# Performance work log

Measured on AMD Instinct MI355X. Metric: run time of the kernel, lower is better.

## Reference

```python
import jax, jax.numpy as jnp
import numpy as np

B, S, D, H, HD, L, V, FF = 4, 2048, 768, 12, 64, 6, 32000, 3072
EPS = 1e-5


def setup_inputs() -> dict:
    key = jax.random.key(0)
    ks = jax.random.split(key, 12)
    s = 0.02
    return {
        "input_ids": jax.random.randint(ks[0], (B, S), 0, V),
        "emb": jax.random.normal(ks[1], (V, D), jnp.float32) * s,
        "q_w": jax.random.normal(ks[2], (L, D, D), jnp.float32) * s,
        "q_b": jnp.zeros((L, D), jnp.float32),
        "k_w": jax.random.normal(ks[3], (L, D, D), jnp.float32) * s,
        "k_b": jnp.zeros((L, D), jnp.float32),
        "v_w": jax.random.normal(ks[4], (L, D, D), jnp.float32) * s,
        "v_b": jnp.zeros((L, D), jnp.float32),
        "o_w": jax.random.normal(ks[5], (L, D, D), jnp.float32) * s,
        "o_b": jnp.zeros((L, D), jnp.float32),
        "f1_w": jax.random.normal(ks[6], (L, D, FF), jnp.float32) * s,
        "f1_b": jnp.zeros((L, FF), jnp.float32),
        "f2_w": jax.random.normal(ks[7], (L, FF, D), jnp.float32) * s,
        "f2_b": jnp.zeros((L, D), jnp.float32),
        "n1_w": jnp.ones((L, D), jnp.float32),
        "n1_b": jnp.zeros((L, D), jnp.float32),
        "n2_w": jnp.ones((L, D), jnp.float32),
        "n2_b": jnp.zeros((L, D), jnp.float32),
        "fn_w": jnp.ones((D,), jnp.float32),
        "fn_b": jnp.zeros((D,), jnp.float32),
    }


def _ln(x, w, b):
    m = jnp.mean(x, axis=-1, keepdims=True)
    v = jnp.var(x, axis=-1, keepdims=True)
    return (x - m) * jax.lax.rsqrt(v + EPS) * w + b


def _rope(x):
    # x: [B, S, D]; RoPE applied on full embed dim (as in source)
    inv_freq = 1.0 / (10000.0 ** (jnp.arange(0, D, 2, dtype=jnp.float32) / D))
    ang = jnp.arange(x.shape[1], dtype=jnp.float32)[:, None] * inv_freq[None, :]  # [S, D/2]
    cos, sin = jnp.cos(ang), jnp.sin(ang)
    xe, xo = x[..., ::2], x[..., 1::2]
    re = xe * cos - xo * sin
    ro = xo * cos + xe * sin
    return jnp.stack([re, ro], axis=-1).reshape(x.shape)


def _forward(input_ids, emb, q_w, q_b, k_w, k_b, v_w, v_b, o_w, o_b,
             f1_w, f1_b, f2_w, f2_b, n1_w, n1_b, n2_w, n2_b, fn_w, fn_b):
    h = _rope(emb[input_ids])  # [B, S, D]
    scale = 1.0 / np.sqrt(HD)

    def block(h, p):
        (qw, qb, kw, kb, vw, vb, ow, ob, f1w, f1b, f2w, f2b,
         w1, b1, w2, b2) = p
        xn = _ln(h, w1, b1)
        q = (xn @ qw + qb).reshape(B, S, H, HD)
        k = (xn @ kw + kb).reshape(B, S, H, HD)
        v = (xn @ vw + vb).reshape(B, S, H, HD)
        scores = jnp.einsum('bqhd,bkhd->bhqk', q, k) * scale
        attn = jax.nn.softmax(scores, axis=-1)
        ctx = jnp.einsum('bhqk,bkhd->bqhd', attn, v).reshape(B, S, D)
        h = h + (ctx @ ow + ob)
        xn2 = _ln(h, w2, b2)
        ff = jax.nn.gelu(xn2 @ f1w + f1b, approximate=False) @ f2w + f2b
        return h + ff, None

    params = (q_w, q_b, k_w, k_b, v_w, v_b, o_w, o_b,
              f1_w, f1_b, f2_w, f2_b, n1_w, n1_b, n2_w, n2_b)
    h, _ = jax.lax.scan(block, h, params)
    h = _ln(h, fn_w, fn_b)
    return h @ emb.T  # tied output projection: [B, S, V]


def reference(input_ids, emb, q_w, q_b, k_w, k_b, v_w, v_b, o_w, o_b,
              f1_w, f1_b, f2_w, f2_b, n1_w, n1_b, n2_w, n2_b, fn_w, fn_b):
    return _forward(input_ids, emb, q_w, q_b, k_w, k_b, v_w, v_b, o_w, o_b,
                    f1_w, f1_b, f2_w, f2_b, n1_w, n1_b, n2_w, n2_b, fn_w, fn_b)
```

## Files before the change

### kernel.cpp

```cpp
#include <hip/hip_runtime.h>
#include <hip/hip_bf16.h>
#include <cstdint>
#include <cstddef>

#define TB 4
#define TS 2048
#define TD 768
#define TH 12
#define THD 64
#define TL 6
#define TV 32000
#define TFF 3072
#define TT (TB*TS)
#define TQKV 2304

typedef __bf16 bf16_t;
typedef __attribute__((ext_vector_type(8))) __bf16 bf16x8;
typedef __attribute__((ext_vector_type(4))) __bf16 bf16x4;
typedef __attribute__((ext_vector_type(4))) float f32x4;

__device__ __forceinline__ unsigned short f2bf(float f) {
  union { float f; unsigned u; } x; x.f = f;
  unsigned r = x.u + 0x7fffu + ((x.u >> 16) & 1u);
  return (unsigned short)(r >> 16);
}

__device__ __forceinline__ float fexp2(float x) {
  float r; asm("v_exp_f32 %0, %1" : "=v"(r) : "v"(x)); return r;
}

__device__ __forceinline__ void gld_lds16(const void* g, void* l) {
  unsigned loff = (unsigned)(uintptr_t)l;
  __builtin_amdgcn_global_load_lds(
      (const __attribute__((address_space(1))) unsigned int*)(uintptr_t)g,
      (__attribute__((address_space(3))) unsigned int*)(uintptr_t)loff, 16, 0, 0);
}

#define IRFENCE() asm volatile("" ::: "memory")

__global__ void embed_rope(const int* __restrict__ ids, const float* __restrict__ emb,
                           float* __restrict__ h) {
  int t = blockIdx.x;
  int s = t & (TS - 1);
  int id = ids[t];
  const float* row = emb + (size_t)id * TD;
  float* out = h + (size_t)t * TD;
  for (int p = threadIdx.x; p < TD/2; p += blockDim.x) {
    float xe = row[2*p], xo = row[2*p+1];
    float inv = expf(-(float)(2*p) * (9.210340371976184f / (float)TD));
    float ang = (float)s * inv;
    float c = cosf(ang), sn = sinf(ang);
    out[2*p]   = xe*c - xo*sn;
    out[2*p+1] = xo*c + xe*sn;
  }
}

__global__ __launch_bounds__(256) void ln_fwd(const float* __restrict__ x,
                                              const float* __restrict__ w,
                                              const float* __restrict__ b,
                                              unsigned short* __restrict__ y) {
  int row = blockIdx.x;
  const float* xr = x + (size_t)row * TD;
  int tid = threadIdx.x;
  float4 v = {0.f, 0.f, 0.f, 0.f};
  if (tid < 192) v = *(const float4*)(xr + tid*4);
  float s = (v.x+v.y)+(v.z+v.w);
  float q = (v.x*v.x+v.y*v.y)+(v.z*v.z+v.w*v.w);
  for (int o = 32; o; o >>= 1) { s += __shfl_down(s, o); q += __shfl_down(q, o); }
  __shared__ float ss[4], sq[4];
  int wave = tid >> 6, lane = tid & 63;
  if (lane == 0) { ss[wave] = s; sq[wave] = q; }
  __syncthreads();
  s = ss[0]+ss[1]+ss[2]+ss[3];
  q = sq[0]+sq[1]+sq[2]+sq[3];
  float mean = s * (1.0f/TD);
  float var  = q * (1.0f/TD) - mean*mean;
  float rstd = rsqrtf(var + 1e-5f);
  if (tid < 192) {
    const float4 wv = *(const float4*)(w + tid*4);
    const float4 bv = *(const float4*)(b + tid*4);
    ushort4 o4;
    o4.x = f2bf((v.x-mean)*rstd*wv.x + bv.x);
    o4.y = f2bf((v.y-mean)*rstd*wv.y + bv.y);
    o4.z = f2bf((v.z-mean)*rstd*wv.z + bv.z);
    o4.w = f2bf((v.w-mean)*rstd*wv.w + bv.w);
    *(ushort4*)(y + (size_t)row*TD + tid*4) = o4;
  }
}

__global__ __launch_bounds__(256) void transpose_to_bf16(const float* __restrict__ W,
                                                         unsigned short* __restrict__ Wt,
                                                         int K, int N, int row_off,
                                                         size_t lstride) {
  int ntn = N / 64;
  int tk = (blockIdx.x / ntn) * 64;
  int tn = (blockIdx.x % ntn) * 64;
  const float* Wb = W + (size_t)blockIdx.y * K * N;
  unsigned short* Ob = Wt + (size_t)blockIdx.y * lstride;
  __shared__ float tile[64][65];
  int tid = threadIdx.x;
  int c = tid & 63, w = tid >> 6;
  #pragma unroll
  for (int i = 0; i < 16; ++i) {
    int r = i*4 + w;
    tile[r][c] = Wb[(size_t)(tk + r) * N + tn + c];
  }
  __syncthreads();
  #pragma unroll
  for (int i = 0; i < 16; ++i) {
    int r = i*4 + w;
    Ob[(size_t)(row_off + tn + r) * K + tk + c] = f2bf(tile[c][r]);
  }
}

__global__ void pack_qkv_bias(const float* __restrict__ qb, const float* __restrict__ kb,
                              const float* __restrict__ vb, float* __restrict__ out) {
  int lay = blockIdx.x, i = threadIdx.x;
  out[lay*TQKV + i]        = qb[lay*TD + i];
  out[lay*TQKV + TD + i]   = kb[lay*TD + i];
  out[lay*TQKV + 2*TD + i] = vb[lay*TD + i];
}

__global__ void convert_bf16_k(const float* __restrict__ in, unsigned short* __restrict__ out) {
  size_t i = ((size_t)blockIdx.x * 256 + threadIdx.x) * 4;
  float4 v = *(const float4*)(in + i);
  ushort4 o;
  o.x = f2bf(v.x); o.y = f2bf(v.y); o.z = f2bf(v.z); o.w = f2bf(v.w);
  *(ushort4*)(out + i) = o;
}

template<int MODE>
__global__ __launch_bounds__(256, 2) void gemm_bt(
    const bf16_t* __restrict__ A, const bf16_t* __restrict__ Bt,
    const float* __restrict__ bias, void* __restrict__ out,
    void* __restrict__ out2,
    int N, int K, int ntn) {
  __shared__ __align__(16) bf16_t As[2][128*64];
  __shared__ __align__(16) bf16_t Bs[2][128*64];
  const int tid = threadIdx.x;
  const int lane = tid & 63;
  const int wave = tid >> 6;
  const int wm = wave >> 1, wn = wave & 1;
  const int nwg = gridDim.x;
  const int orig = blockIdx.x;
  const int qd = nwg >> 3, rr = nwg & 7;
  const int xcd = orig & 7, sub = orig >> 3;
  const int wg = (xcd < rr ? xcd*(qd+1) : rr*(qd+1) + (xcd-rr)*qd) + sub;
  const int tm = wg / ntn, tn = wg % ntn;
  const bf16_t* Ab = A + (size_t)tm * 128 * K;
  const bf16_t* Bb = Bt + (size_t)tn * 128 * K;
  const int lr = lane >> 3;
  const int lc = ((lane & 7) ^ lr) * 8;
  const int l15 = lane & 15, l4 = lane >> 4;
  const int flip = (l15 & 7) << 3;
  const int NT = K >> 6;
  f32x4 acc[4][4] = {};

#define STAGE(t, buf) do {                                                   \
    _Pragma("unroll")                                                        \
    for (int it = 0; it < 4; ++it) {                                         \
      const int r0 = it*32 + wave*8;                                         \
      gld_lds16(Ab + (size_t)(r0 + lr)*K + (t)*64 + lc, &As[buf][r0*64 + lr*64]); \
      gld_lds16(Bb + (size_t)(r0 + lr)*K + (t)*64 + lc, &Bs[buf][r0*64 + lr*64]); \
    }                                                                        \
  } while (0)

  STAGE(0, 0);
  for (int t = 0; t < NT; ++t) {
    const int cur = t & 1;
    if (t < NT - 1) {
      STAGE(t+1, cur^1);
      asm volatile("s_waitcnt vmcnt(8)" ::: "memory");
    } else {
      asm volatile("s_waitcnt vmcnt(0)" ::: "memory");
    }
    IRFENCE(); __builtin_amdgcn_s_barrier(); IRFENCE();
    #pragma unroll
    for (int kh = 0; kh < 2; ++kh) {
      bf16x8 af[4], bfr[4];
      #pragma unroll
      for (int i = 0; i < 4; ++i)
        af[i] = *(const bf16x8*)&As[cur][(wm*64 + i*16 + l15)*64 + ((kh*32 + l4*8) ^ flip)];
      #pragma unroll
      for (int i = 0; i < 4; ++i)
        bfr[i] = *(const bf16x8*)&Bs[cur][(wn*64 + i*16 + l15)*64 + ((kh*32 + l4*8) ^ flip)];
      #pragma unroll
      for (int mi = 0; mi < 4; ++mi)
        #pragma unroll
        for (int ni = 0; ni < 4; ++ni)
          acc[mi][ni] = __builtin_amdgcn_mfma_f32_16x16x32_bf16(af[mi], bfr[ni], acc[mi][ni], 0, 0, 0);
    }
    IRFENCE(); __builtin_amdgcn_s_barrier(); IRFENCE();
  }
#undef STAGE
  const int rb = tm*128 + wm*64 + l4*4;
  const int cbase = tn*128 + wn*64 + l15;
  const bool vsec = (MODE == 4) && (tn >= (2*TD)/128);
  #pragma unroll
  for (int mi = 0; mi < 4; ++mi) {
    #pragma unroll
    for (int ni = 0; ni < 4; ++ni) {
      const int c = cbase + ni*16;
      const float bv = (MODE == 3) ? 0.0f : bias[c];
      if (MODE == 4 && vsec) {
        const int cc = c - 2*TD;
        const int hh = cc >> 6, d = cc & 63;
        const int row0 = rb + mi*16;
        const int bidx = row0 >> 11, s = row0 & (TS-1);
        ushort4 o4;
        o4.x = f2bf(acc[mi][ni][0] + bv);
        o4.y = f2bf(acc[mi][ni][1] + bv);
        o4.z = f2bf(acc[mi][ni][2] + bv);
        o4.w = f2bf(acc[mi][ni][3] + bv);
        *(ushort4*)((unsigned short*)out2 + ((size_t)(bidx*TH + hh)*THD + d)*TS + s) = o4;
        continue;
      }
      #pragma unroll
      for (int r = 0; r < 4; ++r) {
        const size_t idx = (size_t)(rb + mi*16 + r) * N + c;
        float vv = acc[mi][ni][r] + bv;
        if (MODE == 0 || MODE == 4) {
          ((unsigned short*)out)[idx] = f2bf(vv);
        } else if (MODE == 1) {
          vv = 0.5f * vv * (1.0f + erff(vv * 0.70710678118654752f));
          ((unsigned short*)out)[idx] = f2bf(vv);
        } else if (MODE == 2) {
          ((float*)out)[idx] += vv;
        } else {
          ((float*)out)[idx] = vv;
        }
      }
    }
  }
}

__device__ __forceinline__ int lds_half_off(int R, int C) {
  int lin = ((((R >> 4) << 1) | (C >> 5)) << 10) | ((R & 15) << 6) | ((C & 31) << 1);
  return lin ^ (((R >> 3) & 1) << 5);
}

template<int MODE>
__global__ __launch_bounds__(512, 2) void gemm256(
    const bf16_t* __restrict__ A, const bf16_t* __restrict__ Bt,
    const float* __restrict__ bias, void* __restrict__ out,
    int N, int K, int ntn) {
  __shared__ __align__(16) bf16_t lds[2][2][2][8192];
  const int tid = threadIdx.x;
  const int lane = tid & 63;
  const int wave = tid >> 6;
  const int wm = wave >> 2;
  const int wn = wave & 3;
  const int orig = blockIdx.x;
  const int xcd = orig & 7, sub = orig >> 3;
  const int tm = xcd * 4 + (sub & 3);
  const int tn = sub >> 2;
  const bf16_t* Ab = A  + (size_t)tm * 256 * K;
  const bf16_t* Bb = Bt + (size_t)tn * 256 * K;
  const int l15 = lane & 15, l4 = lane >> 4;
  const int s_row = wave*16 + (lane >> 2);
  const int s_col0 = ((lane & 3) * 8) ^ ((lane >= 32) ? 16 : 0);
  const int NT = K >> 6;

  f32x4 acc[2][4][2][2] = {};
  bf16x8 afr[4][2], bfr0[2][2], bfr1[2][2];

#define STAGEH(mat, half, kt, buf) do {                                          \
    const bf16_t* base_ = (mat) ? Bb : Ab;                                       \
    _Pragma("unroll")                                                            \
    for (int j_ = 0; j_ < 2; ++j_)                                               \
      gld_lds16(base_ + (size_t)((half)*128 + s_row)*K + (kt)*64 + j_*32 + s_col0, \
                &lds[buf][mat][half][(wave*2 + j_) * 512]);                      \
  } while (0)
#define RDA(buf, half) do {                                                      \
    _Pragma("unroll")                                                            \
    for (int m4_ = 0; m4_ < 4; ++m4_)                                            \
      _Pragma("unroll")                                                          \
      for (int kh_ = 0; kh_ < 2; ++kh_)                                          \
        afr[m4_][kh_] = *(const bf16x8*)((const char*)&lds[buf][0][half][0] +    \
            lds_half_off(wm*64 + m4_*16 + l15, kh_*32 + l4*8));                  \
  } while (0)
#define RDB(buf, half, dst) do {                                                 \
    _Pragma("unroll")                                                            \
    for (int n2_ = 0; n2_ < 2; ++n2_)                                            \
      _Pragma("unroll")                                                          \
      for (int kh_ = 0; kh_ < 2; ++kh_)                                          \
        dst[n2_][kh_] = *(const bf16x8*)((const char*)&lds[buf][1][half][0] +    \
            lds_half_off(wn*32 + n2_*16 + l15, kh_*32 + l4*8));                  \
  } while (0)
#define MMA(hA, hB, bsrc) do {                                                   \
    __builtin_amdgcn_s_setprio(1);                                               \
    _Pragma("unroll")                                                            \
    for (int m4_ = 0; m4_ < 4; ++m4_)                                            \
      _Pragma("unroll")                                                          \
      for (int n2_ = 0; n2_ < 2; ++n2_)                                          \
        _Pragma("unroll")                                                        \
        for (int kh_ = 0; kh_ < 2; ++kh_)                                        \
          acc[hA][m4_][hB][n2_] = __builtin_amdgcn_mfma_f32_16x16x32_bf16(       \
              afr[m4_][kh_], bsrc[n2_][kh_], acc[hA][m4_][hB][n2_], 0, 0, 0);    \
    __builtin_amdgcn_s_setprio(0);                                               \
  } while (0)
#define WAITV(n)  asm volatile("s_waitcnt vmcnt(" #n ")" ::: "memory")
#define GATE()    do { asm volatile("s_waitcnt lgkmcnt(0)" ::: "memory");        \
                       __builtin_amdgcn_sched_barrier(0); } while (0)
#define BAR()     do { IRFENCE(); __builtin_amdgcn_s_barrier(); IRFENCE(); } while (0)

  STAGEH(0, 0, 0, 0);
  STAGEH(1, 0, 0, 0);
  STAGEH(1, 1, 0, 0);
  STAGEH(0, 1, 0, 0);
  WAITV(4);
  BAR();

  for (int t = 0; t < NT; ++t) {
    const int c = t & 1;
    const bool last = (t == NT - 1);
    RDA(c, 0);
    RDB(c, 0, bfr0);
    if (!last) STAGEH(0, 0, t+1, c^1);
    if (last) WAITV(2); else WAITV(4);
    BAR(); GATE();
    MMA(0, 0, bfr0);
    RDB(c, 1, bfr1);
    if (!last) STAGEH(1, 0, t+1, c^1);
    if (last) WAITV(0); else WAITV(4);
    BAR(); GATE();
    MMA(0, 1, bfr1);
    RDA(c, 1);
    if (!last) STAGEH(1, 1, t+1, c^1);
    BAR(); GATE();
    MMA(1, 0, bfr0);
    if (!last) STAGEH(0, 1, t+1, c^1);
    WAITV(4);
    BAR(); GATE();
    MMA(1, 1, bfr1);
  }

  #pragma unroll
  for (int hA = 0; hA < 2; ++hA)
    #pragma unroll
    for (int m4 = 0; m4 < 4; ++m4) {
      const int row = tm*256 + hA*128 + wm*64 + m4*16 + l4*4;
      #pragma unroll
      for (int hB = 0; hB < 2; ++hB)
        #pragma unroll
        for (int n2 = 0; n2 < 2; ++n2) {
          const int col = tn*256 + hB*128 + wn*32 + n2*16 + l15;
          const float bv = (MODE == 3) ? 0.0f : bias[col];
          #pragma unroll
          for (int r = 0; r < 4; ++r) {
            const size_t idx = (size_t)(row + r) * N + col;
            float vv = acc[hA][m4][hB][n2][r] + bv;
            if (MODE == 0) {
              ((unsigned short*)out)[idx] = f2bf(vv);
            } else if (MODE == 1) {
              vv = 0.5f * vv * (1.0f + erff(vv * 0.70710678118654752f));
              ((unsigned short*)out)[idx] = f2bf(vv);
            } else if (MODE == 2) {
              ((float*)out)[idx] += vv;
            } else {
              ((float*)out)[idx] = vv;
            }
          }
        }
    }
#undef STAGEH
#undef RDA
#undef RDB
#undef MMA
#undef WAITV
#undef GATE
#undef BAR
}

__global__ __launch_bounds__(256) void attn_fwd(
    const bf16_t* __restrict__ xqkv, const bf16_t* __restrict__ vt,
    unsigned short* __restrict__ ctx) {
  __shared__ __align__(16) bf16_t Ks[3][64*64];
  __shared__ __align__(16) bf16_t Vs[3][64*64];
  __shared__ __align__(16) bf16_t pl[4][32*64];
  const int tid = threadIdx.x, lane = tid & 63, wave = tid >> 6;
  const int orig = blockIdx.x;
  const int wg = (orig & 7) * 96 + (orig >> 3);
  const int qb16 = wg & 15;
  const int bh = wg >> 4;
  const int b = bh / TH, h = bh % TH;
  const bf16_t* qp = xqkv + (size_t)b*TS*TQKV + h*THD;
  const bf16_t* kp = xqkv + (size_t)b*TS*TQKV + TD + h*THD;
  const bf16_t* vp = vt + (size_t)bh*THD*TS;
  const int l15 = lane & 15, l4 = lane >> 4;
  const int qrow0 = qb16*128 + wave*32;
  const float C1 = 0.18033688011112042f;
  bf16x8 qf[2][2];
  #pragma unroll
  for (int mi = 0; mi < 2; ++mi)
    #pragma unroll
    for (int kh = 0; kh < 2; ++kh)
      qf[mi][kh] = *(const bf16x8*)(qp + (size_t)(qrow0 + mi*16 + l15)*TQKV + kh*32 + l4*8);
  const int srow = lane >> 3;
  const int scol = ((lane & 7) ^ srow) * 8;
  f32x4 o[2][4] = {};
  float rm[2] = {-1e30f, -1e30f}, rl[2] = {0.0f, 0.0f};
  const int flipw = (l15 & 7) << 3;

  #define STAGE(t, buf) do {                                                     \
    _Pragma("unroll")                                                            \
    for (int i_ = 0; i_ < 2; ++i_) {                                             \
      const int r_ = i_*32 + wave*8;                                             \
      gld_lds16(kp + (size_t)((t)*64 + r_ + srow)*TQKV + scol, &Ks[buf][r_*64]); \
      gld_lds16(vp + (size_t)(r_ + srow)*TS + (t)*64 + scol,   &Vs[buf][r_*64]); \
    }                                                                            \
  } while (0)

  STAGE(0, 0);
  STAGE(1, 1);
  int cur = 0;
  for (int t = 0; t < TS/64; ++t) {
    if (t < TS/64 - 1) {
      asm volatile("s_waitcnt vmcnt(4)" ::: "memory");
    } else {
      asm volatile("s_waitcnt vmcnt(0)" ::: "memory");
    }
    IRFENCE(); __builtin_amdgcn_s_barrier(); IRFENCE();
    if (t + 2 < TS/64) {
      const int nb = (cur + 2 >= 3) ? cur - 1 : cur + 2;
      STAGE(t+2, nb);
    }
    bf16x8 kf[4][2];
    #pragma unroll
    for (int nj = 0; nj < 4; ++nj) {
      const int row = nj*16 + l15;
      const int flip = (row & 7) << 3;
      #pragma unroll
      for (int kh = 0; kh < 2; ++kh)
        kf[nj][kh] = *(const bf16x8*)&Ks[cur][row*64 + ((kh*32 + l4*8) ^ flip)];
    }
    f32x4 st[2][4] = {};
    #pragma unroll
    for (int mi = 0; mi < 2; ++mi)
      #pragma unroll
      for (int nj = 0; nj < 4; ++nj) {
        st[mi][nj] = __builtin_amdgcn_mfma_f32_16x16x32_bf16(kf[nj][0], qf[mi][0], st[mi][nj], 0, 0, 0);
        st[mi][nj] = __builtin_amdgcn_mfma_f32_16x16x32_bf16(kf[nj][1], qf[mi][1], st[mi][nj], 0, 0, 0);
      }
    float mx[2];
    #pragma unroll
    for (int mi = 0; mi < 2; ++mi) {
      float m0 = fmaxf(fmaxf(st[mi][0][0], st[mi][0][1]), fmaxf(st[mi][0][2], st[mi][0][3]));
      float m1 = fmaxf(fmaxf(st[mi][1][0], st[mi][1][1]), fmaxf(st[mi][1][2], st[mi][1][3]));
      float m2 = fmaxf(fmaxf(st[mi][2][0], st[mi][2][1]), fmaxf(st[mi][2][2], st[mi][2][3]));
      float m3 = fmaxf(fmaxf(st[mi][3][0], st[mi][3][1]), fmaxf(st[mi][3][2], st[mi][3][3]));
      float m = fmaxf(fmaxf(m0, m1), fmaxf(m2, m3)) * C1;
      m = fmaxf(m, __shfl_xor(m, 16));
      m = fmaxf(m, __shfl_xor(m, 32));
      mx[mi] = m;
    }
    float worst = fmaxf(mx[0] - rm[0], mx[1] - rm[1]);
    if (!__all(worst <= 11.54f)) {
      #pragma unroll
      for (int mi = 0; mi < 2; ++mi) {
        float mn = fmaxf(rm[mi], mx[mi]);
        float sc = fexp2(rm[mi] - mn);
        rm[mi] = mn;
        rl[mi] *= sc;
        #pragma unroll
        for (int r = 0; r < 4; ++r) {
          float scr = __shfl(sc, l4*4 + r, 16);
          #pragma unroll
          for (int df = 0; df < 4; ++df) o[mi][df][r] *= scr;
        }
      }
    }
    #pragma unroll
    for (int mi = 0; mi < 2; ++mi) {
      float rs = 0.0f;
      #pragma unroll
      for (int nj = 0; nj < 4; ++nj) {
        float p0 = fexp2(st[mi][nj][0]*C1 - rm[mi]);
        float p1 = fexp2(st[mi][nj][1]*C1 - rm[mi]);
        float p2 = fexp2(st[mi][nj][2]*C1 - rm[mi]);
        float p3 = fexp2(st[mi][nj][3]*C1 - rm[mi]);
        rs += (p0+p1)+(p2+p3);
        bf16x4 pk;
        pk[0] = (bf16_t)p0; pk[1] = (bf16_t)p1; pk[2] = (bf16_t)p2; pk[3] = (bf16_t)p3;
        const int colb = (nj*16 + l4*4) ^ flipw;
        *(bf16x4*)(&pl[wave][(mi*16 + l15)*64 + colb]) = pk;
      }
      rs += __shfl_xor(rs, 16);
      rs += __shfl_xor(rs, 32);
      rl[mi] += rs;
    }
    bf16x8 pa[2][2], vf[4][2];
    #pragma unroll
    for (int mi = 0; mi < 2; ++mi) {
      #pragma unroll
      for (int ks = 0; ks < 2; ++ks)
        pa[mi][ks] = *(const bf16x8*)&pl[wave][(mi*16 + l15)*64 + ((ks*32 + l4*8) ^ flipw)];
    }
    #pragma unroll
    for (int df = 0; df < 4; ++df) {
      const int vrow = df*16 + l15;
      const int flip = (vrow & 7) << 3;
      #pragma unroll
      for (int ks = 0; ks < 2; ++ks)
        vf[df][ks] = *(const bf16x8*)&Vs[cur][vrow*64 + ((ks*32 + l4*8) ^ flip)];
    }
    #pragma unroll
    for (int mi = 0; mi < 2; ++mi)
      #pragma unroll
      for (int df = 0; df < 4; ++df) {
        o[mi][df] = __builtin_amdgcn_mfma_f32_16x16x32_bf16(pa[mi][0], vf[df][0], o[mi][df], 0, 0, 0);
        o[mi][df] = __builtin_amdgcn_mfma_f32_16x16x32_bf16(pa[mi][1], vf[df][1], o[mi][df], 0, 0, 0);
      }
    cur = (cur + 1 >= 3) ? 0 : cur + 1;
  }
  #undef STAGE
  #pragma unroll
  for (int mi = 0; mi < 2; ++mi) {
    const float inv = 1.0f / rl[mi];
    #pragma unroll
    for (int r = 0; r < 4; ++r) {
      const float invr = __shfl(inv, l4*4 + r, 16);
      const size_t rowoff = (size_t)b*TS*TD + (size_t)(qrow0 + mi*16 + l4*4 + r)*TD + h*THD;
      #pragma unroll
      for (int df = 0; df < 4; ++df)
        ctx[rowoff + df*16 + l15] = f2bf(o[mi][df][r] * invr);
    }
  }
}

extern "C" void kernel_launch(void* const* d_in, const int* in_sizes, int n_in,
                              void* d_out, int out_size, void* d_ws, size_t ws_size,
                              hipStream_t stream) {
  (void)in_sizes; (void)n_in; (void)out_size;
  const int*   ids  = (const int*)  d_in[0];
  const float* emb  = (const float*)d_in[1];
  const float* q_w  = (const float*)d_in[2];
  const float* q_b  = (const float*)d_in[3];
  const float* k_w  = (const float*)d_in[4];
  const float* k_b  = (const float*)d_in[5];
  const float* v_w  = (const float*)d_in[6];
  const float* v_b  = (const float*)d_in[7];
  const float* o_w  = (const float*)d_in[8];
  const float* o_b  = (const float*)d_in[9];
  const float* f1_w = (const float*)d_in[10];
  const float* f1_b = (const float*)d_in[11];
  const float* f2_w = (const float*)d_in[12];
  const float* f2_b = (const float*)d_in[13];
  const float* n1_w = (const float*)d_in[14];
  const float* n1_b = (const float*)d_in[15];
  const float* n2_w = (const float*)d_in[16];
  const float* n2_b = (const float*)d_in[17];
  const float* fn_w = (const float*)d_in[18];
  const float* fn_b = (const float*)d_in[19];

  char* ws = (char*)d_ws;
  size_t off = 0;
  auto alloc = [&](size_t bytes) -> void* {
    void* p = ws + off;
    off += (bytes + 255) & ~(size_t)255;
    return p;
  };
  float*          h    = (float*)         alloc((size_t)TT*TD*4);
  unsigned short* xn   = (unsigned short*)alloc((size_t)TT*TD*2);
  unsigned short* xqkv = (unsigned short*)alloc((size_t)TT*TQKV*2);
  unsigned short* cb   = (unsigned short*)alloc((size_t)TT*TD*2);
  unsigned short* ffb  = (unsigned short*)alloc((size_t)TT*TFF*2);
  unsigned short* wqkv = (unsigned short*)alloc((size_t)TL*TQKV*TD*2);
  unsigned short* wot  = (unsigned short*)alloc((size_t)TL*TD*TD*2);
  unsigned short* wf1t = (unsigned short*)alloc((size_t)TL*TD*TFF*2);
  unsigned short* wf2t = (unsigned short*)alloc((size_t)TL*TD*TFF*2);
  unsigned short* embb = (unsigned short*)alloc((size_t)TV*TD*2);
  float*          bqkv = (float*)         alloc((size_t)TL*TQKV*4);
  if (off > ws_size) return;
  bf16_t* vt = (bf16_t*)ffb;

  transpose_to_bf16<<<dim3((TD/64)*(TD/64), TL), 256, 0, stream>>>(q_w, wqkv, TD, TD, 0,    (size_t)TQKV*TD);
  transpose_to_bf16<<<dim3((TD/64)*(TD/64), TL), 256, 0, stream>>>(k_w, wqkv, TD, TD, TD,   (size_t)TQKV*TD);
  transpose_to_bf16<<<dim3((TD/64)*(TD/64), TL), 256, 0, stream>>>(v_w, wqkv, TD, TD, 2*TD, (size_t)TQKV*TD);
  transpose_to_bf16<<<dim3((TD/64)*(TD/64), TL), 256, 0, stream>>>(o_w, wot, TD, TD, 0, (size_t)TD*TD);
  transpose_to_bf16<<<dim3((TD/64)*(TFF/64), TL), 256, 0, stream>>>(f1_w, wf1t, TD, TFF, 0, (size_t)TD*TFF);
  transpose_to_bf16<<<dim3((TFF/64)*(TD/64), TL), 256, 0, stream>>>(f2_w, wf2t, TFF, TD, 0, (size_t)TD*TFF);
  pack_qkv_bias<<<TL, TD, 0, stream>>>(q_b, k_b, v_b, bqkv);
  convert_bf16_k<<<(TV*TD)/1024, 256, 0, stream>>>(emb, embb);
  embed_rope<<<TT, 256, 0, stream>>>(ids, emb, h);

  for (int lay = 0; lay < TL; ++lay) {
    ln_fwd<<<TT, 256, 0, stream>>>(h, n1_w + lay*TD, n1_b + lay*TD, xn);
    gemm_bt<4><<<(TT/128)*(TQKV/128), 256, 0, stream>>>((const bf16_t*)xn,
        (const bf16_t*)(wqkv + (size_t)lay*TQKV*TD), bqkv + lay*TQKV, xqkv, vt, TQKV, TD, TQKV/128);
    attn_fwd<<<TB*TH*(TS/128), 256, 0, stream>>>((const bf16_t*)xqkv, vt, cb);
    gemm_bt<2><<<(TT/128)*(TD/128), 256, 0, stream>>>((const bf16_t*)cb,
        (const bf16_t*)(wot + (size_t)lay*TD*TD), o_b + lay*TD, h, nullptr, TD, TD, TD/128);
    ln_fwd<<<TT, 256, 0, stream>>>(h, n2_w + lay*TD, n2_b + lay*TD, xn);
    gemm_bt<1><<<(TT/128)*(TFF/128), 256, 0, stream>>>((const bf16_t*)xn,
        (const bf16_t*)(wf1t + (size_t)lay*TD*TFF), f1_b + lay*TFF, ffb, nullptr, TFF, TD, TFF/128);
    gemm_bt<2><<<(TT/128)*(TD/128), 256, 0, stream>>>((const bf16_t*)ffb,
        (const bf16_t*)(wf2t + (size_t)lay*TD*TFF), f2_b + lay*TD, h, nullptr, TD, TFF, TD/128);
  }
  ln_fwd<<<TT, 256, 0, stream>>>(h, fn_w, fn_b, xn);
  gemm256<3><<<32*(TV/256), 512, 0, stream>>>((const bf16_t*)xn,
      (const bf16_t*)embb, nullptr, d_out, TV, TD, TV/256);
}
```

Measured before the change: 2.495 ms.

## Shrink attention LDS to double buffer, raise occupancy, remap GEMM tile order

The attention kernel drops from triple to double buffering of K/V tiles and halves the per-wave probability scratch by reusing one 16-row slice per mi. K and V fragments are loaded and consumed inside the MFMA loops to cut live registers, and launch bounds request 4 blocks per CU. A second barrier is added per iteration to protect the shared double buffer, and prefetch depth drops from two tiles to one. The GEMM block-to-tile mapping changes from an XCD-aware swizzle to grouped column-major ordering, which may affect L2 locality.

```diff
diff --git a/kernel.cpp b/kernel.cpp
--- a/kernel.cpp
+++ b/kernel.cpp
@@ -251,9 +251,10 @@
   const int wm = wave >> 2;
   const int wn = wave & 3;
   const int orig = blockIdx.x;
-  const int xcd = orig & 7, sub = orig >> 3;
-  const int tm = xcd * 4 + (sub & 3);
-  const int tn = sub >> 2;
+  const int grp = orig >> 8;
+  const int rem = orig & 255;
+  const int tn = grp*8 + (rem >> 5);
+  const int tm = rem & 31;
   const bf16_t* Ab = A  + (size_t)tm * 256 * K;
   const bf16_t* Bb = Bt + (size_t)tn * 256 * K;
   const int l15 = lane & 15, l4 = lane >> 4;
@@ -372,12 +373,12 @@
 #undef BAR
 }
 
-__global__ __launch_bounds__(256) void attn_fwd(
+__global__ __launch_bounds__(256, 4) void attn_fwd(
     const bf16_t* __restrict__ xqkv, const bf16_t* __restrict__ vt,
     unsigned short* __restrict__ ctx) {
-  __shared__ __align__(16) bf16_t Ks[3][64*64];
-  __shared__ __align__(16) bf16_t Vs[3][64*64];
-  __shared__ __align__(16) bf16_t pl[4][32*64];
+  __shared__ __align__(16) bf16_t Ks[2][64*64];
+  __shared__ __align__(16) bf16_t Vs[2][64*64];
+  __shared__ __align__(16) bf16_t pl[4][16*64];
   const int tid = threadIdx.x, lane = tid & 63, wave = tid >> 6;
   const int orig = blockIdx.x;
   const int wg = (orig & 7) * 96 + (orig >> 3);
@@ -412,36 +413,27 @@
   } while (0)
 
   STAGE(0, 0);
-  STAGE(1, 1);
-  int cur = 0;
   for (int t = 0; t < TS/64; ++t) {
+    const int cur = t & 1;
     if (t < TS/64 - 1) {
+      STAGE(t+1, cur^1);
       asm volatile("s_waitcnt vmcnt(4)" ::: "memory");
     } else {
       asm volatile("s_waitcnt vmcnt(0)" ::: "memory");
     }
     IRFENCE(); __builtin_amdgcn_s_barrier(); IRFENCE();
-    if (t + 2 < TS/64) {
-      const int nb = (cur + 2 >= 3) ? cur - 1 : cur + 2;
-      STAGE(t+2, nb);
-    }
-    bf16x8 kf[4][2];
+    f32x4 st[2][4] = {};
     #pragma unroll
     for (int nj = 0; nj < 4; ++nj) {
       const int row = nj*16 + l15;
       const int flip = (row & 7) << 3;
-      #pragma unroll
-      for (int kh = 0; kh < 2; ++kh)
-        kf[nj][kh] = *(const bf16x8*)&Ks[cur][row*64 + ((kh*32 + l4*8) ^ flip)];
-    }
-    f32x4 st[2][4] = {};
-    #pragma unroll
-    for (int mi = 0; mi < 2; ++mi)
-      #pragma unroll
-      for (int nj = 0; nj < 4; ++nj) {
-        st[mi][nj] = __builtin_amdgcn_mfma_f32_16x16x32_bf16(kf[nj][0], qf[mi][0], st[mi][nj], 0, 0, 0);
-        st[mi][nj] = __builtin_amdgcn_mfma_f32_16x16x32_bf16(kf[nj][1], qf[mi][1], st[mi][nj], 0, 0, 0);
-      }
+      bf16x8 kf0 = *(const bf16x8*)&Ks[cur][row*64 + ((l4*8) ^ flip)];
+      bf16x8 kf1 = *(const bf16x8*)&Ks[cur][row*64 + ((32 + l4*8) ^ flip)];
+      st[0][nj] = __builtin_amdgcn_mfma_f32_16x16x32_bf16(kf0, qf[0][0], st[0][nj], 0, 0, 0);
+      st[0][nj] = __builtin_amdgcn_mfma_f32_16x16x32_bf16(kf1, qf[0][1], st[0][nj], 0, 0, 0);
+      st[1][nj] = __builtin_amdgcn_mfma_f32_16x16x32_bf16(kf0, qf[1][0], st[1][nj], 0, 0, 0);
+      st[1][nj] = __builtin_amdgcn_mfma_f32_16x16x32_bf16(kf1, qf[1][1], st[1][nj], 0, 0, 0);
+    }
     float mx[2];
     #pragma unroll
     for (int mi = 0; mi < 2; ++mi) {
@@ -470,6 +462,7 @@
         }
       }
     }
+    bf16x8 pa[2][2];
     #pragma unroll
     for (int mi = 0; mi < 2; ++mi) {
       float rs = 0.0f;
@@ -483,35 +476,26 @@
         bf16x4 pk;
         pk[0] = (bf16_t)p0; pk[1] = (bf16_t)p1; pk[2] = (bf16_t)p2; pk[3] = (bf16_t)p3;
         const int colb = (nj*16 + l4*4) ^ flipw;
-        *(bf16x4*)(&pl[wave][(mi*16 + l15)*64 + colb]) = pk;
+        *(bf16x4*)(&pl[wave][l15*64 + colb]) = pk;
       }
       rs += __shfl_xor(rs, 16);
       rs += __shfl_xor(rs, 32);
       rl[mi] += rs;
-    }
-    bf16x8 pa[2][2], vf[4][2];
-    #pragma unroll
-    for (int mi = 0; mi < 2; ++mi) {
-      #pragma unroll
-      for (int ks = 0; ks < 2; ++ks)
-        pa[mi][ks] = *(const bf16x8*)&pl[wave][(mi*16 + l15)*64 + ((ks*32 + l4*8) ^ flipw)];
+      pa[mi][0] = *(const bf16x8*)&pl[wave][l15*64 + ((l4*8) ^ flipw)];
+      pa[mi][1] = *(const bf16x8*)&pl[wave][l15*64 + ((32 + l4*8) ^ flipw)];
     }
     #pragma unroll
     for (int df = 0; df < 4; ++df) {
       const int vrow = df*16 + l15;
       const int flip = (vrow & 7) << 3;
-      #pragma unroll
-      for (int ks = 0; ks < 2; ++ks)
-        vf[df][ks] = *(const bf16x8*)&Vs[cur][vrow*64 + ((ks*32 + l4*8) ^ flip)];
-    }
-    #pragma unroll
-    for (int mi = 0; mi < 2; ++mi)
-      #pragma unroll
-      for (int df = 0; df < 4; ++df) {
-        o[mi][df] = __builtin_amdgcn_mfma_f32_16x16x32_bf16(pa[mi][0], vf[df][0], o[mi][df], 0, 0, 0);
-        o[mi][df] = __builtin_amdgcn_mfma_f32_16x16x32_bf16(pa[mi][1], vf[df][1], o[mi][df], 0, 0, 0);
-      }
-    cur = (cur + 1 >= 3) ? 0 : cur + 1;
+      bf16x8 vf0 = *(const bf16x8*)&Vs[cur][vrow*64 + ((l4*8) ^ flip)];
+      bf16x8 vf1 = *(const bf16x8*)&Vs[cur][vrow*64 + ((32 + l4*8) ^ flip)];
+      o[0][df] = __builtin_amdgcn_mfma_f32_16x16x32_bf16(pa[0][0], vf0, o[0][df], 0, 0, 0);
+      o[0][df] = __builtin_amdgcn_mfma_f32_16x16x32_bf16(pa[0][1], vf1, o[0][df], 0, 0, 0);
+      o[1][df] = __builtin_amdgcn_mfma_f32_16x16x32_bf16(pa[1][0], vf0, o[1][df], 0, 0, 0);
+      o[1][df] = __builtin_amdgcn_mfma_f32_16x16x32_bf16(pa[1][1], vf1, o[1][df], 0, 0, 0);
+    }
+    IRFENCE(); __builtin_amdgcn_s_barrier(); IRFENCE();
   }
   #undef STAGE
   #pragma unroll
```

Measured after the change: 2.427 ms. 2.7% less time.
